# Optimization experiments

Measured on AMD Instinct MI355X. Metric: run time of the kernel, lower is better.

Reference implementation:

```python
import jax, jax.numpy as jnp
import numpy as np

EPS = 1e-5


def _lstm(x, W_ih, W_hh, b_ih, b_hh):
    # x: [B, T, in]; torch LSTM gate order i, f, g, o. Returns (last h, last c).
    def step(carry, xt):
        h, c = carry
        z = xt @ W_ih.T + h @ W_hh.T + (b_ih + b_hh)  # [B, 4H]
        i, f, g, o = jnp.split(z, 4, axis=-1)
        c = jax.nn.sigmoid(f) * c + jax.nn.sigmoid(i) * jnp.tanh(g)
        h = jax.nn.sigmoid(o) * jnp.tanh(c)
        return (h, c), None
    h0 = jnp.zeros((x.shape[0], W_hh.shape[1]), x.dtype)
    (h, c), _ = jax.lax.scan(step, (h0, h0), jnp.swapaxes(x, 0, 1))
    return h, c


def _bn_train(x, g, b):
    # BatchNorm1d in training mode: batch stats, biased variance.
    m = x.mean(axis=0)
    v = x.var(axis=0)
    return g * (x - m) * jax.lax.rsqrt(v + EPS) + b


def _forward(agent_traj, neighbours, aW_ih, aW_hh, ab_ih, ab_hh,
             nW_ih, nW_hh, nb_ih, nb_hh, dW_ih, dW_hh, db_ih, db_hh,
             pW, pb, rW, rb, m1W, m1b, g1, be1, m2W, m2b, g2, be2,
             i1W, i1b, ig1, ib1, i2W, i2b, ig2, ib2, segment_ids):
    B = agent_traj.shape[0]
    # relative distance: neighbour last position - owning agent's last position
    rel = neighbours[:, -1, :] - agent_traj[segment_ids, -1, :]          # [N, 2]
    agent_h, agent_c = _lstm(agent_traj, aW_ih, aW_hh, ab_ih, ab_hh)     # [B, 64]
    neigh_h, _ = _lstm(neighbours, nW_ih, nW_hh, nb_ih, nb_hh)           # [N, 64]
    rel_emb = rel @ rW.T + rb                                            # [N, 64]
    x = jnp.concatenate([neigh_h, rel_emb], axis=1)                      # [N, 128]
    x = _bn_train(jax.nn.relu(x @ m1W.T + m1b), g1, be1)                 # [N, 512]
    x = _bn_train(jax.nn.relu(x @ m2W.T + m2b), g2, be2)                 # [N, 1024]
    # per-sample max pooling over each sample's neighbours (zeros if none)
    pooled = jax.ops.segment_max(x, segment_ids, num_segments=B)         # [B, 1024]
    counts = jax.ops.segment_sum(jnp.ones((x.shape[0],), x.dtype), segment_ids, num_segments=B)
    pooled = jnp.where(counts[:, None] > 0, pooled, jnp.zeros((), x.dtype))
    d = jnp.concatenate([pooled, agent_h], axis=1)                       # [B, 1088]
    d = _bn_train(jax.nn.relu(d @ i1W.T + i1b), ig1, ib1)                # [B, 1024]
    d = _bn_train(jax.nn.relu(d @ i2W.T + i2b), ig2, ib2)                # [B, 64]

    def dec_step(carry, _):
        h, c = carry
        z = h @ dW_ih.T + h @ dW_hh.T + (db_ih + db_hh)
        i, f, g, o = jnp.split(z, 4, axis=-1)
        c = jax.nn.sigmoid(f) * c + jax.nn.sigmoid(i) * jnp.tanh(g)
        h = jax.nn.sigmoid(o) * jnp.tanh(c)
        return (h, c), h
    _, hs = jax.lax.scan(dec_step, (d, agent_c), None, length=30)        # [30, B, 64]
    pred = jnp.einsum('tbh,oh->bto', hs, pW) + pb                        # [B, 30, 2]
    return pred


def setup_inputs() -> dict:
    B, T, N, Tn, H = 2048, 20, 32768, 20, 64
    key = jax.random.key(0)
    ki = iter(jax.random.split(key, 40))
    def rn(shape, s=0.1):
        return jax.random.normal(next(ki), shape, dtype=jnp.float32) * s
    inp = dict(
        agent_traj=rn((B, T, 2), 1.0),
        neighbours=rn((N, Tn, 2), 1.0),
        aW_ih=rn((4 * H, 2)), aW_hh=rn((4 * H, H)), ab_ih=rn((4 * H,)), ab_hh=rn((4 * H,)),
        nW_ih=rn((4 * H, 2)), nW_hh=rn((4 * H, H)), nb_ih=rn((4 * H,)), nb_hh=rn((4 * H,)),
        dW_ih=rn((4 * H, H)), dW_hh=rn((4 * H, H)), db_ih=rn((4 * H,)), db_hh=rn((4 * H,)),
        pW=rn((2, H)), pb=rn((2,)),
        rW=rn((H, 2)), rb=rn((H,)),
        m1W=rn((512, 128)), m1b=rn((512,)),
        g1=jnp.ones((512,), jnp.float32), be1=jnp.zeros((512,), jnp.float32),
        m2W=rn((1024, 512)), m2b=rn((1024,)),
        g2=jnp.ones((1024,), jnp.float32), be2=jnp.zeros((1024,), jnp.float32),
        i1W=rn((1024, 1088)), i1b=rn((1024,)),
        ig1=jnp.ones((1024,), jnp.float32), ib1=jnp.zeros((1024,), jnp.float32),
        i2W=rn((H, 1024)), i2b=rn((H,)),
        ig2=jnp.ones((H,), jnp.float32), ib2=jnp.zeros((H,), jnp.float32),
        segment_ids=jnp.sort(jax.random.randint(next(ki), (N,), 0, B)).astype(jnp.int32),
    )
    return inp


def reference(agent_traj, neighbours, aW_ih, aW_hh, ab_ih, ab_hh,
              nW_ih, nW_hh, nb_ih, nb_hh, dW_ih, dW_hh, db_ih, db_hh,
              pW, pb, rW, rb, m1W, m1b, g1, be1, m2W, m2b, g2, be2,
              i1W, i1b, ig1, ib1, i2W, i2b, ig2, ib2, segment_ids):
    return _forward(agent_traj, neighbours, aW_ih, aW_hh, ab_ih, ab_hh,
                    nW_ih, nW_hh, nb_ih, nb_hh, dW_ih, dW_hh, db_ih, db_hh,
                    pW, pb, rW, rb, m1W, m1b, g1, be1, m2W, m2b, g2, be2,
                    i1W, i1b, ig1, ib1, i2W, i2b, ig2, ib2, segment_ids)
```

## Files before the change

### kernel.cpp

```cpp
#include <hip/hip_runtime.h>

#define EPS_BN 1e-5f

typedef __attribute__((ext_vector_type(8))) short short8;
typedef __attribute__((ext_vector_type(4))) float f32x4;

__device__ __forceinline__ float fast_rcp(float x) { return __builtin_amdgcn_rcpf(x); }
__device__ __forceinline__ float sigmoid_f(float x) { return fast_rcp(1.0f + __expf(-x)); }
__device__ __forceinline__ float tanh_f(float x) { return 1.0f - 2.0f * fast_rcp(__expf(2.0f * x) + 1.0f); }

__device__ __forceinline__ unsigned short f2bf(float f) {
    unsigned u = __float_as_uint(f);
    u += 0x7FFFu + ((u >> 16) & 1u);
    return (unsigned short)(u >> 16);
}
__device__ __forceinline__ unsigned pk_bf(float a, float b) {
    return (unsigned)f2bf(a) | ((unsigned)f2bf(b) << 16);
}
__device__ __forceinline__ float bf_hi(float f) {
    return __uint_as_float((unsigned)f2bf(f) << 16);
}
__device__ __forceinline__ float bf2f(unsigned short u) {
    return __uint_as_float((unsigned)u << 16);
}

union AFrag { short e[8]; short8 v; };
union BFrag { uint4 u; short8 v; };

__global__ __launch_bounds__(256, 2) void lstm_mfma(
    const float* __restrict__ x,
    const float* __restrict__ W_ih,
    const float* __restrict__ W_hh,
    const float* __restrict__ b_ih,
    const float* __restrict__ b_hh,
    float* __restrict__ h_out,
    float* __restrict__ c_out,
    int T)
{
    __shared__ unsigned h_ex[2][16 * 52];
    __shared__ float z_lds[4 * 64 * 17];

    const int tid  = threadIdx.x;
    const int g    = tid >> 6;
    const int lane = tid & 63;
    const int s    = lane & 15;
    const int q    = lane >> 4;

    short8 ahi[4][3], alo[4][3];
#pragma unroll
    for (int Ti = 0; Ti < 4; ++Ti) {
        const int n = g * 64 + Ti * 16 + s;
#pragma unroll
        for (int kc = 0; kc < 2; ++kc) {
            const float* src = &W_hh[n * 64 + kc * 32 + q * 8];
            float4 v0 = *(const float4*)src;
            float4 v1 = *(const float4*)(src + 4);
            float v[8] = {v0.x, v0.y, v0.z, v0.w, v1.x, v1.y, v1.z, v1.w};
            AFrag a, b;
#pragma unroll
            for (int j = 0; j < 8; ++j) {
                a.e[j] = (short)f2bf(v[j]);
                b.e[j] = (short)f2bf(v[j] - bf_hi(v[j]));
            }
            ahi[Ti][kc] = a.v;
            alo[Ti][kc] = b.v;
        }
        AFrag a2, b2;
#pragma unroll
        for (int j = 0; j < 8; ++j) { a2.e[j] = 0; b2.e[j] = 0; }
        if (q == 0) {
            const float wi0 = W_ih[n * 2 + 0];
            const float wi1 = W_ih[n * 2 + 1];
            const float bs  = b_ih[n] + b_hh[n];
            a2.e[0] = (short)f2bf(wi0); b2.e[0] = (short)f2bf(wi0 - bf_hi(wi0));
            a2.e[1] = (short)f2bf(wi1); b2.e[1] = (short)f2bf(wi1 - bf_hi(wi1));
            a2.e[2] = (short)f2bf(bs);  b2.e[2] = (short)f2bf(bs  - bf_hi(bs));
        }
        ahi[Ti][2] = a2.v;
        alo[Ti][2] = b2.v;
    }

    for (int i = tid; i < 2 * 16 * 52; i += 256) (&h_ex[0][0])[i] = 0u;
    __syncthreads();
    if (tid < 16) {
        h_ex[0][tid * 52 + 33] = pk_bf(1.0f, 0.0f);
        float2 xv = *(const float2*)&x[((long)blockIdx.x * 16 + tid) * (long)(T * 2)];
        h_ex[0][tid * 52 + 32] = pk_bf(xv.x, xv.y);
        h_ex[1][tid * 52 + 32] = pk_bf(xv.x - bf_hi(xv.x), xv.y - bf_hi(xv.y));
    }
    __syncthreads();

    const int jg = tid >> 4;
    const int sc = tid & 15;
    const long seqc = (long)blockIdx.x * 16 + sc;
    float creg[4] = {0.f, 0.f, 0.f, 0.f};

    for (int t = 0; t < T; ++t) {
        BFrag bhi[3], blo[3];
#pragma unroll
        for (int kc = 0; kc < 3; ++kc) {
            const int off = s * 52 + kc * 16 + (q >> 1) * 8 + (q & 1) * 4;
            bhi[kc].u = *(const uint4*)&h_ex[0][off];
            blo[kc].u = *(const uint4*)&h_ex[1][off];
        }

        f32x4 acc[4];
#pragma unroll
        for (int Ti = 0; Ti < 4; ++Ti) acc[Ti] = (f32x4)0.f;

#pragma unroll
        for (int kc = 0; kc < 3; ++kc) {
            const short8 bh = bhi[kc].v;
            const short8 bl = blo[kc].v;
#pragma unroll
            for (int Ti = 0; Ti < 4; ++Ti) {
                f32x4 a = acc[Ti];
                a = __builtin_amdgcn_mfma_f32_16x16x32_bf16(ahi[Ti][kc], bh, a, 0, 0, 0);
                a = __builtin_amdgcn_mfma_f32_16x16x32_bf16(ahi[Ti][kc], bl, a, 0, 0, 0);
                a = __builtin_amdgcn_mfma_f32_16x16x32_bf16(alo[Ti][kc], bh, a, 0, 0, 0);
                acc[Ti] = a;
            }
        }

#pragma unroll
        for (int Ti = 0; Ti < 4; ++Ti)
#pragma unroll
        for (int r = 0; r < 4; ++r)
            z_lds[(g * 64 + Ti * 16 + q * 4 + r) * 17 + s] = acc[Ti][r];
        __syncthreads();

        float hval[4];
#pragma unroll
        for (int r = 0; r < 4; ++r) {
            const int j = jg * 4 + r;
            const float zi = z_lds[(0 * 64 + j) * 17 + sc];
            const float zf = z_lds[(1 * 64 + j) * 17 + sc];
            const float zg = z_lds[(2 * 64 + j) * 17 + sc];
            const float zo = z_lds[(3 * 64 + j) * 17 + sc];
            const float c = fmaf(sigmoid_f(zf), creg[r], sigmoid_f(zi) * tanh_f(zg));
            creg[r] = c;
            hval[r] = sigmoid_f(zo) * tanh_f(c);
        }
        {
            const int j0 = jg * 4;
            const int w0 = sc * 52 + (j0 >> 4) * 8 + ((j0 >> 2) & 3) * 2;
            h_ex[0][w0]     = pk_bf(hval[0], hval[1]);
            h_ex[0][w0 + 1] = pk_bf(hval[2], hval[3]);
            h_ex[1][w0]     = pk_bf(hval[0] - bf_hi(hval[0]), hval[1] - bf_hi(hval[1]));
            h_ex[1][w0 + 1] = pk_bf(hval[2] - bf_hi(hval[2]), hval[3] - bf_hi(hval[3]));
        }
        if (tid < 16 && t + 1 < T) {
            float2 xv = *(const float2*)&x[((long)blockIdx.x * 16 + tid) * (long)(T * 2) + (t + 1) * 2];
            h_ex[0][tid * 52 + 32] = pk_bf(xv.x, xv.y);
            h_ex[1][tid * 52 + 32] = pk_bf(xv.x - bf_hi(xv.x), xv.y - bf_hi(xv.y));
        }
        if (t == T - 1) {
#pragma unroll
            for (int r = 0; r < 4; ++r) {
                h_out[seqc * 64 + jg * 4 + r] = hval[r];
                if (c_out) c_out[seqc * 64 + jg * 4 + r] = creg[r];
            }
        }
        __syncthreads();
    }
}

__global__ __launch_bounds__(256) void build_x0(
    const float* __restrict__ neigh_h, const float* __restrict__ neighbours,
    const float* __restrict__ agent_traj, const int* __restrict__ seg,
    const float* __restrict__ rW, const float* __restrict__ rb,
    unsigned short* __restrict__ x0hi, unsigned short* __restrict__ x0lo, int T)
{
    const long n = (long)blockIdx.x * 2 + (threadIdx.x >> 7);
    const int j = threadIdx.x & 127;
    float v;
    if (j < 64) {
        v = neigh_h[n*64 + j];
    } else {
        const int o = j - 64;
        const int sid = seg[n];
        const float ra = neighbours[n*(long)(T*2) + (T-1)*2 + 0] - agent_traj[(long)sid*(T*2) + (T-1)*2 + 0];
        const float rbv= neighbours[n*(long)(T*2) + (T-1)*2 + 1] - agent_traj[(long)sid*(T*2) + (T-1)*2 + 1];
        v = fmaf(rW[o*2+0], ra, fmaf(rW[o*2+1], rbv, rb[o]));
    }
    x0hi[n*128 + j] = f2bf(v);
    x0lo[n*128 + j] = f2bf(v - bf_hi(v));
}

__global__ __launch_bounds__(64) void prep_wfrag(
    const float* __restrict__ W, const float* __restrict__ sc, int K,
    unsigned short* __restrict__ Whi, unsigned short* __restrict__ Wlo)
{
    const int nKc = K >> 5;
    const int blk = blockIdx.x;
    const int ti = blk / nKc, kc = blk - ti * nKc;
    const int l = threadIdx.x;
    const int n = ti * 16 + (l & 15);
    const int k0 = kc * 32 + (l >> 4) * 8;
    const long ob = ((long)blk * 64 + l) * 8;
#pragma unroll
    for (int j = 0; j < 8; ++j) {
        float v = W[(long)n * K + k0 + j];
        if (sc) v *= sc[k0 + j];
        Whi[ob + j] = f2bf(v);
        Wlo[ob + j] = f2bf(v - bf_hi(v));
    }
}

__global__ __launch_bounds__(64) void prep_bias(
    const float* __restrict__ W, const float* __restrict__ sh,
    const float* __restrict__ b, int K, float* __restrict__ bout)
{
    const int n = blockIdx.x;
    const int l = threadIdx.x;
    float s = 0.f;
    if (sh)
        for (int k = l; k < K; k += 64) s += sh[k] * W[(long)n * K + k];
#pragma unroll
    for (int m = 32; m >= 1; m >>= 1) s += __shfl_xor(s, m, 64);
    if (l == 0) bout[n] = b[n] + s;
}

__global__ __launch_bounds__(256, 2) void gemm_split(
    const unsigned short* __restrict__ Ahi,
    const unsigned short* __restrict__ Alo,
    const unsigned short* __restrict__ Whi,
    const unsigned short* __restrict__ Wlo,
    const float* __restrict__ bias,
    float* __restrict__ Yf,
    unsigned short* __restrict__ Yhi,
    unsigned short* __restrict__ Ylo,
    float* __restrict__ accum,
    const int* __restrict__ segp,
    float* __restrict__ poolmax,
    int M, int K, int O)
{
    __shared__ unsigned short As[2][2][128 * 56];
    __shared__ int segl[128];
    const int t = threadIdx.x;
    const int lane = t & 63;
    const int w = t >> 6;
    const int wm = w & 1, wn = w >> 1;

    const int nx = gridDim.x;
    const int flat = blockIdx.y * nx + blockIdx.x;
    const int grp = flat / (8 * nx);
    const int loc = flat - grp * (8 * nx);
    const int m0 = (grp * 8 + (loc & 7)) * 128;
    const int n0 = (loc >> 3) * 128;
    const int nKc = K >> 5;

    f32x4 acc[4][4];
#pragma unroll
    for (int mt = 0; mt < 4; ++mt)
#pragma unroll
    for (int nt = 0; nt < 4; ++nt) acc[mt][nt] = (f32x4)0.f;

    const long aoff = (long)(m0 + (t >> 1)) * K + (t & 1) * 16;
    const unsigned short* aph = Ahi + aoff;
    const unsigned short* apl = Alo + aoff;
    const int so = (t >> 1) * 56 + (t & 1) * 16;
    const int arow = wm * 64 + (lane & 15);
    const int acol = (lane >> 4) * 8;
    const long bt0 = (long)((n0 >> 4) + wn * 4);

    uint4 rah0, rah1, ral0, ral1;
    auto loadAreg = [&](int kc) {
        rah0 = *(const uint4*)(aph + kc * 32);
        rah1 = *(const uint4*)(aph + kc * 32 + 8);
        ral0 = *(const uint4*)(apl + kc * 32);
        ral1 = *(const uint4*)(apl + kc * 32 + 8);
    };
    auto storeAs = [&](int buf) {
        *(uint4*)&As[buf][0][so] = rah0; *(uint4*)&As[buf][0][so + 8] = rah1;
        *(uint4*)&As[buf][1][so] = ral0; *(uint4*)&As[buf][1][so + 8] = ral1;
    };
    auto loadB = [&](BFrag* bh, BFrag* bl, int kc) {
#pragma unroll
        for (int nt = 0; nt < 4; ++nt) {
            const long fb = ((bt0 + nt) * nKc + kc) * 512 + lane * 8;
            bh[nt].u = *(const uint4*)(Whi + fb);
            bl[nt].u = *(const uint4*)(Wlo + fb);
        }
    };
    auto compute = [&](int buf, BFrag* bh, BFrag* bl) {
        BFrag afh[4], afl[4];
#pragma unroll
        for (int mt = 0; mt < 4; ++mt) {
            afh[mt].u = *(const uint4*)&As[buf][0][(arow + mt * 16) * 56 + acol];
            afl[mt].u = *(const uint4*)&As[buf][1][(arow + mt * 16) * 56 + acol];
        }
#pragma unroll
        for (int nt = 0; nt < 4; ++nt)
#pragma unroll
        for (int mt = 0; mt < 4; ++mt) {
            f32x4 a = acc[mt][nt];
            a = __builtin_amdgcn_mfma_f32_16x16x32_bf16(afh[mt].v, bh[nt].v, a, 0, 0, 0);
            a = __builtin_amdgcn_mfma_f32_16x16x32_bf16(afh[mt].v, bl[nt].v, a, 0, 0, 0);
            a = __builtin_amdgcn_mfma_f32_16x16x32_bf16(afl[mt].v, bh[nt].v, a, 0, 0, 0);
            acc[mt][nt] = a;
        }
    };

    BFrag bh0[4], bl0[4], bh1[4], bl1[4];
    loadAreg(0);
    loadB(bh0, bl0, 0);
    storeAs(0);
    __syncthreads();
    for (int kc = 0; kc < nKc; kc += 2) {
        loadAreg(kc + 1);
        loadB(bh1, bl1, kc + 1);
        compute(0, bh0, bl0);
        storeAs(1);
        __syncthreads();
        if (kc + 2 < nKc) {
            loadAreg(kc + 2);
            loadB(bh0, bl0, kc + 2);
        }
        compute(1, bh1, bl1);
        if (kc + 2 < nKc) {
            storeAs(0);
            __syncthreads();
        }
    }

    if (segp) {
        __syncthreads();
        if (t < 128) segl[t] = segp[m0 + t];
        __syncthreads();
    }

    const int cn = lane & 15, cq = lane >> 4;
#pragma unroll
    for (int nt = 0; nt < 4; ++nt) {
        const int n = n0 + wn * 64 + nt * 16 + cn;
        const float bs = bias[n];
        float s = 0.f, ssq = 0.f;
#pragma unroll
        for (int mt = 0; mt < 4; ++mt) {
            const int mb = wm * 64 + mt * 16 + cq * 4;
            float vmax = 0.f; int sid = -1;
#pragma unroll
            for (int r = 0; r < 4; ++r) {
                const float v = fmaxf(acc[mt][nt][r] + bs, 0.f);
                s += v; ssq += v * v;
                if (segp) {
                    const int sr = segl[mb + r];
                    if (r == 0) { vmax = v; sid = sr; }
                    else if (sr == sid) { vmax = fmaxf(vmax, v); }
                    else {
                        if (vmax > 0.f)
                            atomicMax((int*)&poolmax[(long)sid * O + n], __float_as_int(vmax));
                        sid = sr; vmax = v;
                    }
                } else if (Yf) {
                    Yf[(long)(m0 + mb + r) * O + n] = v;
                } else {
                    const long idx = (long)(m0 + mb + r) * O + n;
                    Yhi[idx] = f2bf(v);
                    Ylo[idx] = f2bf(v - bf_hi(v));
                }
            }
            if (segp && vmax > 0.f)
                atomicMax((int*)&poolmax[(long)sid * O + n], __float_as_int(vmax));
        }
        if (accum) {
            s   += __shfl_xor(s, 16, 64);   ssq += __shfl_xor(ssq, 16, 64);
            s   += __shfl_xor(s, 32, 64);   ssq += __shfl_xor(ssq, 32, 64);
            if (cq == 0) {
                atomicAdd(&accum[n], s);
                atomicAdd(&accum[O + n], ssq);
            }
        }
    }
}

__global__ __launch_bounds__(256) void colstats(
    const float* __restrict__ Y, int M, int O, int chunkRows,
    float* __restrict__ accum)
{
    const int c = blockIdx.x * 64 + (threadIdx.x & 63);
    const int rgrp = threadIdx.x >> 6;
    const int r0 = blockIdx.y * chunkRows;
    int rend = r0 + chunkRows; if (rend > M) rend = M;
    float s = 0.f, ss = 0.f;
    for (int r = r0 + rgrp; r < rend; r += 4) {
        const float v = Y[(long)r*O + c];
        s += v; ss += v*v;
    }
    __shared__ float l1[256], l2[256];
    l1[threadIdx.x] = s; l2[threadIdx.x] = ss;
    __syncthreads();
    if (threadIdx.x < 64) {
        const int c2 = blockIdx.x * 64 + threadIdx.x;
        s  = l1[threadIdx.x] + l1[threadIdx.x+64] + l1[threadIdx.x+128] + l1[threadIdx.x+192];
        ss = l2[threadIdx.x] + l2[threadIdx.x+64] + l2[threadIdx.x+128] + l2[threadIdx.x+192];
        atomicAdd(&accum[c2], s);
        atomicAdd(&accum[O + c2], ss);
    }
}

__global__ __launch_bounds__(256) void bn_finalize(
    const float* __restrict__ accum, const float* __restrict__ g,
    const float* __restrict__ be, int O, float invM,
    float* __restrict__ scale, float* __restrict__ shift)
{
    const int o = blockIdx.x * 256 + threadIdx.x;
    if (o < O) {
        const float mean = accum[o] * invM;
        const float var  = accum[O + o] * invM - mean * mean;
        const float sc   = g[o] * rsqrtf(var + EPS_BN);
        scale[o] = sc;
        shift[o] = be[o] - mean * sc;
    }
}

__global__ __launch_bounds__(256) void build_d0(
    const float* __restrict__ poolraw, const float* __restrict__ agent_h,
    const int* __restrict__ seg, int N,
    const float* __restrict__ sc2, const float* __restrict__ sh2,
    unsigned short* __restrict__ d0hi, unsigned short* __restrict__ d0lo)
{
    const int b = blockIdx.x;
    int l = 0, h = N;
    while (l < h) { const int mid = (l + h) >> 1; if (seg[mid] < b) l = mid + 1; else h = mid; }
    const bool nonempty = (l < N) && (seg[l] == b);
    for (int c = threadIdx.x; c < 1088; c += 256) {
        float v;
        if (c < 1024) {
            v = nonempty ? fmaf(sc2[c], poolraw[(long)b*1024 + c], sh2[c]) : 0.f;
        } else {
            v = agent_h[(long)b*64 + (c - 1024)];
        }
        d0hi[(long)b*1088 + c] = f2bf(v);
        d0lo[(long)b*1088 + c] = f2bf(v - bf_hi(v));
    }
}

__global__ __launch_bounds__(256) void gemm_i2_part(
    const float* __restrict__ A,
    const float* __restrict__ W,
    const float* __restrict__ ascale, const float* __restrict__ ashift,
    float* __restrict__ part, int M, int K, int kchunk)
{
    __shared__ float As[16][132];
    __shared__ float Bs[16][68];
    const int t = threadIdx.x;
    const int m0 = blockIdx.x * 128;
    const int ks = blockIdx.y;
    const int kbeg = ks * kchunk;
    const int kend = kbeg + kchunk;
    const int tm = (t & 15) * 8;
    const int tn = (t >> 4) * 4;
    const int ar = t >> 1;
    const int ac = (t & 1) * 8;
    const int br = t >> 2;
    const int bc = (t & 3) * 4;

    float acc[8][4];
#pragma unroll
    for (int i = 0; i < 8; ++i)
#pragma unroll
    for (int j = 0; j < 4; ++j) acc[i][j] = 0.f;

    for (int k0 = kbeg; k0 < kend; k0 += 16) {
        float4 a0 = *(const float4*)&A[(long)(m0+ar)*K + k0 + ac];
        float4 a1 = *(const float4*)&A[(long)(m0+ar)*K + k0 + ac + 4];
        float4 s0 = *(const float4*)&ascale[k0 + ac];
        float4 s1 = *(const float4*)&ascale[k0 + ac + 4];
        float4 h0 = *(const float4*)&ashift[k0 + ac];
        float4 h1 = *(const float4*)&ashift[k0 + ac + 4];
        a0.x = fmaf(a0.x, s0.x, h0.x); a0.y = fmaf(a0.y, s0.y, h0.y);
        a0.z = fmaf(a0.z, s0.z, h0.z); a0.w = fmaf(a0.w, s0.w, h0.w);
        a1.x = fmaf(a1.x, s1.x, h1.x); a1.y = fmaf(a1.y, s1.y, h1.y);
        a1.z = fmaf(a1.z, s1.z, h1.z); a1.w = fmaf(a1.w, s1.w, h1.w);
        float4 b0 = *(const float4*)&W[(long)br*K + k0 + bc];
        __syncthreads();
        As[ac+0][ar] = a0.x; As[ac+1][ar] = a0.y; As[ac+2][ar] = a0.z; As[ac+3][ar] = a0.w;
        As[ac+4][ar] = a1.x; As[ac+5][ar] = a1.y; As[ac+6][ar] = a1.z; As[ac+7][ar] = a1.w;
        Bs[bc+0][br] = b0.x; Bs[bc+1][br] = b0.y; Bs[bc+2][br] = b0.z; Bs[bc+3][br] = b0.w;
        __syncthreads();
#pragma unroll
        for (int kk = 0; kk < 16; ++kk) {
            float av[8], bv[4];
            *(float4*)&av[0] = *(const float4*)&As[kk][tm];
            *(float4*)&av[4] = *(const float4*)&As[kk][tm + 4];
            *(float4*)&bv[0] = *(const float4*)&Bs[kk][tn];
#pragma unroll
            for (int i = 0; i < 8; ++i)
#pragma unroll
            for (int j = 0; j < 4; ++j)
                acc[i][j] = fmaf(av[i], bv[j], acc[i][j]);
        }
    }

    float* po = part + (long)ks * M * 64;
#pragma unroll
    for (int i = 0; i < 8; ++i)
        *(float4*)&po[(long)(m0 + tm + i) * 64 + tn] = *(float4*)&acc[i][0];
}

__global__ __launch_bounds__(256) void i2_finish(
    const float* __restrict__ part, const float* __restrict__ bias,
    int M, int KS, float* __restrict__ t2)
{
    const long idx = (long)blockIdx.x * 256 + threadIdx.x;
    if (idx < (long)M * 64) {
        float s = 0.f;
        for (int ks = 0; ks < KS; ++ks) s += part[(long)ks * M * 64 + idx];
        t2[idx] = fmaxf(s + bias[idx & 63], 0.f);
    }
}

__global__ __launch_bounds__(256) void prep_dec(
    const float* __restrict__ dW_ih, const float* __restrict__ dW_hh,
    const float* __restrict__ db_ih, const float* __restrict__ db_hh,
    float* __restrict__ Wc, float* __restrict__ bc)
{
    const int idx = blockIdx.x * 256 + threadIdx.x;
    if (idx < 256*64) Wc[idx] = dW_ih[idx] + dW_hh[idx];
    else if (idx < 256*64 + 256) bc[idx - 256*64] = db_ih[idx - 256*64] + db_hh[idx - 256*64];
}

__global__ __launch_bounds__(256) void decoder_kernel(
    const float* __restrict__ t2, const float* __restrict__ sc4,
    const float* __restrict__ sh4, const float* __restrict__ agent_c,
    const float* __restrict__ Wc, const float* __restrict__ bc,
    const float* __restrict__ pW, const float* __restrict__ pb,
    float* __restrict__ pred )
{
    __shared__ float h_lds[2][64];
    __shared__ float zg_lds[2][64];
    __shared__ float zo_lds[2][64];
    const int t = threadIdx.x;
    const int lane = t & 63;
    const int wave = t >> 6;
    const int s = wave >> 1;
    const int role = wave & 1;
    const long seq = (long)blockIdx.x * 2 + s;

    const int r0 = role * 128 + lane;
    const int r1 = r0 + 64;
    float w0[64], w1[64];
#pragma unroll
    for (int k = 0; k < 64; k += 4) {
        float4 va = *(const float4*)&Wc[r0 * 64 + k];
        w0[k] = va.x; w0[k+1] = va.y; w0[k+2] = va.z; w0[k+3] = va.w;
        float4 vb = *(const float4*)&Wc[r1 * 64 + k];
        w1[k] = vb.x; w1[k+1] = vb.y; w1[k+2] = vb.z; w1[k+3] = vb.w;
    }
    const float bias0 = bc[r0];
    const float bias1 = bc[r1];
    const float pw0 = pW[lane], pw1 = pW[64 + lane];
    const float pb0 = pb[0], pb1 = pb[1];

    float c = agent_c[seq*64 + lane];
    if (role == 0)
        h_lds[s][lane] = fmaf(sc4[lane], t2[seq*64 + lane], sh4[lane]);
    __syncthreads();
    float hv = h_lds[s][lane];

    for (int step = 0; step < 30; ++step) {
        float z0 = bias0, z1 = bias1;
#pragma unroll
        for (int k = 0; k < 64; ++k) {
            float hk = __int_as_float(__builtin_amdgcn_readlane(__float_as_int(hv), k));
            z0 = fmaf(hk, w0[k], z0);
            z1 = fmaf(hk, w1[k], z1);
        }
        if (role == 1) { zg_lds[s][lane] = z0; zo_lds[s][lane] = z1; }
        __syncthreads();
        if (role == 0) {
            const float ig = sigmoid_f(z0);
            const float fg = sigmoid_f(z1);
            const float gg = tanh_f(zg_lds[s][lane]);
            const float og = sigmoid_f(zo_lds[s][lane]);
            c = fmaf(fg, c, ig * gg);
            h_lds[s][lane] = og * tanh_f(c);
        }
        __syncthreads();
        hv = h_lds[s][lane];
        if (role == 0) {
            float p0 = hv * pw0;
            float p1 = hv * pw1;
#pragma unroll
            for (int m = 32; m >= 1; m >>= 1) {
                p0 += __shfl_xor(p0, m, 64);
                p1 += __shfl_xor(p1, m, 64);
            }
            if (lane == 0) {
                pred[seq*60 + step*2 + 0] = p0 + pb0;
                pred[seq*60 + step*2 + 1] = p1 + pb1;
            }
        }
    }
}

extern "C" void kernel_launch(void* const* d_in, const int* in_sizes, int n_in,
                              void* d_out, int out_size, void* d_ws, size_t ws_size,
                              hipStream_t stream)
{
    const float* agent_traj = (const float*)d_in[0];
    const float* neighbours = (const float*)d_in[1];
    const float* aW_ih = (const float*)d_in[2];
    const float* aW_hh = (const float*)d_in[3];
    const float* ab_ih = (const float*)d_in[4];
    const float* ab_hh = (const float*)d_in[5];
    const float* nW_ih = (const float*)d_in[6];
    const float* nW_hh = (const float*)d_in[7];
    const float* nb_ih = (const float*)d_in[8];
    const float* nb_hh = (const float*)d_in[9];
    const float* dW_ih = (const float*)d_in[10];
    const float* dW_hh = (const float*)d_in[11];
    const float* db_ih = (const float*)d_in[12];
    const float* db_hh = (const float*)d_in[13];
    const float* pW = (const float*)d_in[14];
    const float* pb = (const float*)d_in[15];
    const float* rW = (const float*)d_in[16];
    const float* rb = (const float*)d_in[17];
    const float* m1W = (const float*)d_in[18];
    const float* m1b = (const float*)d_in[19];
    const float* g1  = (const float*)d_in[20];
    const float* be1 = (const float*)d_in[21];
    const float* m2W = (const float*)d_in[22];
    const float* m2b = (const float*)d_in[23];
    const float* g2  = (const float*)d_in[24];
    const float* be2 = (const float*)d_in[25];
    const float* i1W = (const float*)d_in[26];
    const float* i1b = (const float*)d_in[27];
    const float* ig1 = (const float*)d_in[28];
    const float* ib1 = (const float*)d_in[29];
    const float* i2W = (const float*)d_in[30];
    const float* i2b = (const float*)d_in[31];
    const float* ig2 = (const float*)d_in[32];
    const float* ib2 = (const float*)d_in[33];
    const int*   seg = (const int*)d_in[34];
    float* pred = (float*)d_out;

    const int B = 2048, T = 20, N = 32768;

    char* p = (char*)d_ws;
    auto alloc = [&](size_t bytes) -> char* {
        char* r = p; p += (bytes + 255) & ~(size_t)255; return r;
    };
    float* agent_h = (float*)alloc((size_t)B*64*4);
    float* agent_c = (float*)alloc((size_t)B*64*4);
    char* neigh_region = alloc((size_t)N*64*4);
    unsigned short* x0hi = (unsigned short*)alloc((size_t)N*128*2);
    unsigned short* x0lo = (unsigned short*)alloc((size_t)N*128*2);
    char* y1hi_region  = alloc((size_t)N*512*2);
    unsigned short* y1lo = (unsigned short*)alloc((size_t)N*512*2);
    float* poolraw = (float*)alloc((size_t)B*1024*4);
    float* accAll = (float*)alloc((size_t)(1024+2048+2048+128)*4);
    float* acc1 = accAll;
    float* acc2 = accAll + 1024;
    float* acc3 = accAll + 3072;
    float* acc4 = accAll + 5120;
    float* sc1 = (float*)alloc(512*4);  float* sh1 = (float*)alloc(512*4);
    float* sc2 = (float*)alloc(1024*4); float* sh2 = (float*)alloc(1024*4);
    float* sc3 = (float*)alloc(1024*4); float* sh3 = (float*)alloc(1024*4);
    float* sc4 = (float*)alloc(64*4);   float* sh4 = (float*)alloc(64*4);
    float* Wc = (float*)alloc(256*64*4);
    float* bc = (float*)alloc(256*4);
    unsigned short* W1hi = (unsigned short*)alloc((size_t)512*128*2);
    unsigned short* W1lo = (unsigned short*)alloc((size_t)512*128*2);
    unsigned short* W2hi = (unsigned short*)alloc((size_t)1024*512*2);
    unsigned short* W2lo = (unsigned short*)alloc((size_t)1024*512*2);
    unsigned short* Wi1hi = (unsigned short*)alloc((size_t)1024*1088*2);
    unsigned short* Wi1lo = (unsigned short*)alloc((size_t)1024*1088*2);
    float* b1f = (float*)alloc(512*4);
    float* b2f = (float*)alloc(1024*4);
    float* bi1f = (float*)alloc(1024*4);
    float* i2part = (float*)alloc((size_t)8*B*64*4);

    float* neigh_h = (float*)neigh_region;
    float* t1      = (float*)neigh_region;
    unsigned short* y1hi = (unsigned short*)y1hi_region;
    unsigned short* d0hi = (unsigned short*)y1hi_region;
    unsigned short* d0lo = d0hi + (size_t)B*1088;
    float* t2 = (float*)(y1hi_region + (size_t)2*B*1088*2);

    hipMemsetAsync(accAll, 0, (1024+2048+2048+128)*sizeof(float), stream);
    hipMemsetAsync(poolraw, 0, (size_t)B*1024*4, stream);

    prep_wfrag<<<(512/16)*(128/32), 64, 0, stream>>>(m1W, nullptr, 128, W1hi, W1lo);
    prep_bias<<<512, 64, 0, stream>>>(m1W, nullptr, m1b, 128, b1f);
    prep_wfrag<<<(1024/16)*(1088/32), 64, 0, stream>>>(i1W, nullptr, 1088, Wi1hi, Wi1lo);
    prep_bias<<<1024, 64, 0, stream>>>(i1W, nullptr, i1b, 1088, bi1f);
    prep_dec<<<65, 256, 0, stream>>>(dW_ih, dW_hh, db_ih, db_hh, Wc, bc);

    lstm_mfma<<<B/16, 256, 0, stream>>>(agent_traj, aW_ih, aW_hh, ab_ih, ab_hh,
                                        agent_h, agent_c, T);
    lstm_mfma<<<N/16, 256, 0, stream>>>(neighbours, nW_ih, nW_hh, nb_ih, nb_hh,
                                        neigh_h, nullptr, T);
    build_x0<<<N/2, 256, 0, stream>>>(neigh_h, neighbours, agent_traj, seg, rW, rb,
                                      x0hi, x0lo, T);

    gemm_split<<<dim3(512/128, N/128), 256, 0, stream>>>(
        x0hi, x0lo, W1hi, W1lo, b1f, nullptr, y1hi, y1lo, acc1,
        nullptr, nullptr, N, 128, 512);
    bn_finalize<<<2, 256, 0, stream>>>(acc1, g1, be1, 512, 1.0f/N, sc1, sh1);

    prep_wfrag<<<(1024/16)*(512/32), 64, 0, stream>>>(m2W, sc1, 512, W2hi, W2lo);
    prep_bias<<<1024, 64, 0, stream>>>(m2W, sh1, m2b, 512, b2f);

    gemm_split<<<dim3(1024/128, N/128), 256, 0, stream>>>(
        y1hi, y1lo, W2hi, W2lo, b2f, nullptr, nullptr, nullptr, acc2,
        seg, poolraw, N, 512, 1024);
    bn_finalize<<<4, 256, 0, stream>>>(acc2, g2, be2, 1024, 1.0f/N, sc2, sh2);

    build_d0<<<B, 256, 0, stream>>>(poolraw, agent_h, seg, N, sc2, sh2, d0hi, d0lo);

    gemm_split<<<dim3(1024/128, B/128), 256, 0, stream>>>(
        d0hi, d0lo, Wi1hi, Wi1lo, bi1f, t1, nullptr, nullptr, acc3,
        nullptr, nullptr, B, 1088, 1024);
    bn_finalize<<<4, 256, 0, stream>>>(acc3, ig1, ib1, 1024, 1.0f/B, sc3, sh3);

    gemm_i2_part<<<dim3(B/128, 8), 256, 0, stream>>>(t1, i2W, sc3, sh3, i2part,
                                                     B, 1024, 128);
    i2_finish<<<(B*64)/256, 256, 0, stream>>>(i2part, i2b, B, 8, t2);
    colstats<<<dim3(1, 8), 256, 0, stream>>>(t2, B, 64, 256, acc4);
    bn_finalize<<<1, 256, 0, stream>>>(acc4, ig2, ib2, 64, 1.0f/B, sc4, sh4);

    decoder_kernel<<<B/2, 256, 0, stream>>>(t2, sc4, sh4, agent_c, Wc, bc, pW, pb, pred);
}
```

Before: 648.5 us.

## Remap LSTM gate rows per wave to drop LDS z-exchange and barrier

Reassigns weight rows so each wave owns the i, f, g and o gate rows for the same 16 hidden units. The cell update can then be computed directly from MFMA accumulators, with no round trip through z_lds and no __syncthreads. The h exchange buffer is double-buffered, so only one barrier per timestep remains, and the final h/c stores become float4. The aim is to cut LDS traffic and synchronisation on the serial recurrence critical path, at the cost of doubling the h_ex buffer.

```diff
diff --git a/kernel.cpp b/kernel.cpp
--- a/kernel.cpp
+++ b/kernel.cpp
@@ -37,19 +37,18 @@
     float* __restrict__ c_out,
     int T)
 {
-    __shared__ unsigned h_ex[2][16 * 52];
-    __shared__ float z_lds[4 * 64 * 17];
+    __shared__ unsigned h_ex[2][2][16 * 52];
 
     const int tid  = threadIdx.x;
-    const int g    = tid >> 6;
+    const int w    = tid >> 6;
     const int lane = tid & 63;
     const int s    = lane & 15;
     const int q    = lane >> 4;
 
     short8 ahi[4][3], alo[4][3];
 #pragma unroll
-    for (int Ti = 0; Ti < 4; ++Ti) {
-        const int n = g * 64 + Ti * 16 + s;
+    for (int gt = 0; gt < 4; ++gt) {
+        const int n = gt * 64 + w * 16 + s;
 #pragma unroll
         for (int kc = 0; kc < 2; ++kc) {
             const float* src = &W_hh[n * 64 + kc * 32 + q * 8];
@@ -62,8 +61,8 @@
                 a.e[j] = (short)f2bf(v[j]);
                 b.e[j] = (short)f2bf(v[j] - bf_hi(v[j]));
             }
-            ahi[Ti][kc] = a.v;
-            alo[Ti][kc] = b.v;
+            ahi[gt][kc] = a.v;
+            alo[gt][kc] = b.v;
         }
         AFrag a2, b2;
 #pragma unroll
@@ -76,90 +75,77 @@
             a2.e[1] = (short)f2bf(wi1); b2.e[1] = (short)f2bf(wi1 - bf_hi(wi1));
             a2.e[2] = (short)f2bf(bs);  b2.e[2] = (short)f2bf(bs  - bf_hi(bs));
         }
-        ahi[Ti][2] = a2.v;
-        alo[Ti][2] = b2.v;
-    }
-
-    for (int i = tid; i < 2 * 16 * 52; i += 256) (&h_ex[0][0])[i] = 0u;
+        ahi[gt][2] = a2.v;
+        alo[gt][2] = b2.v;
+    }
+
+    for (int i = tid; i < 2 * 2 * 16 * 52; i += 256) (&h_ex[0][0][0])[i] = 0u;
     __syncthreads();
     if (tid < 16) {
-        h_ex[0][tid * 52 + 33] = pk_bf(1.0f, 0.0f);
+        h_ex[0][0][tid * 52 + 33] = pk_bf(1.0f, 0.0f);
+        h_ex[1][0][tid * 52 + 33] = pk_bf(1.0f, 0.0f);
         float2 xv = *(const float2*)&x[((long)blockIdx.x * 16 + tid) * (long)(T * 2)];
-        h_ex[0][tid * 52 + 32] = pk_bf(xv.x, xv.y);
-        h_ex[1][tid * 52 + 32] = pk_bf(xv.x - bf_hi(xv.x), xv.y - bf_hi(xv.y));
+        h_ex[0][0][tid * 52 + 32] = pk_bf(xv.x, xv.y);
+        h_ex[0][1][tid * 52 + 32] = pk_bf(xv.x - bf_hi(xv.x), xv.y - bf_hi(xv.y));
     }
     __syncthreads();
 
-    const int jg = tid >> 4;
-    const int sc = tid & 15;
-    const long seqc = (long)blockIdx.x * 16 + sc;
     float creg[4] = {0.f, 0.f, 0.f, 0.f};
 
     for (int t = 0; t < T; ++t) {
+        const int rb = t & 1, wb = rb ^ 1;
         BFrag bhi[3], blo[3];
 #pragma unroll
         for (int kc = 0; kc < 3; ++kc) {
             const int off = s * 52 + kc * 16 + (q >> 1) * 8 + (q & 1) * 4;
-            bhi[kc].u = *(const uint4*)&h_ex[0][off];
-            blo[kc].u = *(const uint4*)&h_ex[1][off];
+            bhi[kc].u = *(const uint4*)&h_ex[rb][0][off];
+            blo[kc].u = *(const uint4*)&h_ex[rb][1][off];
         }
 
         f32x4 acc[4];
 #pragma unroll
-        for (int Ti = 0; Ti < 4; ++Ti) acc[Ti] = (f32x4)0.f;
+        for (int gt = 0; gt < 4; ++gt) acc[gt] = (f32x4)0.f;
 
 #pragma unroll
         for (int kc = 0; kc < 3; ++kc) {
             const short8 bh = bhi[kc].v;
             const short8 bl = blo[kc].v;
 #pragma unroll
-            for (int Ti = 0; Ti < 4; ++Ti) {
-                f32x4 a = acc[Ti];
-                a = __builtin_amdgcn_mfma_f32_16x16x32_bf16(ahi[Ti][kc], bh, a, 0, 0, 0);
-                a = __builtin_amdgcn_mfma_f32_16x16x32_bf16(ahi[Ti][kc], bl, a, 0, 0, 0);
-                a = __builtin_amdgcn_mfma_f32_16x16x32_bf16(alo[Ti][kc], bh, a, 0, 0, 0);
-                acc[Ti] = a;
+            for (int gt = 0; gt < 4; ++gt) {
+                f32x4 a = acc[gt];
+                a = __builtin_amdgcn_mfma_f32_16x16x32_bf16(ahi[gt][kc], bh, a, 0, 0, 0);
+                a = __builtin_amdgcn_mfma_f32_16x16x32_bf16(ahi[gt][kc], bl, a, 0, 0, 0);
+                a = __builtin_amdgcn_mfma_f32_16x16x32_bf16(alo[gt][kc], bh, a, 0, 0, 0);
+                acc[gt] = a;
             }
         }
 
-#pragma unroll
-        for (int Ti = 0; Ti < 4; ++Ti)
-#pragma unroll
-        for (int r = 0; r < 4; ++r)
-            z_lds[(g * 64 + Ti * 16 + q * 4 + r) * 17 + s] = acc[Ti][r];
-        __syncthreads();
-
         float hval[4];
 #pragma unroll
         for (int r = 0; r < 4; ++r) {
-            const int j = jg * 4 + r;
-            const float zi = z_lds[(0 * 64 + j) * 17 + sc];
-            const float zf = z_lds[(1 * 64 + j) * 17 + sc];
-            const float zg = z_lds[(2 * 64 + j) * 17 + sc];
-            const float zo = z_lds[(3 * 64 + j) * 17 + sc];
-            const float c = fmaf(sigmoid_f(zf), creg[r], sigmoid_f(zi) * tanh_f(zg));
+            const float c = fmaf(sigmoid_f(acc[1][r]), creg[r],
+                                 sigmoid_f(acc[0][r]) * tanh_f(acc[2][r]));
             creg[r] = c;
-            hval[r] = sigmoid_f(zo) * tanh_f(c);
+            hval[r] = sigmoid_f(acc[3][r]) * tanh_f(c);
         }
         {
-            const int j0 = jg * 4;
-            const int w0 = sc * 52 + (j0 >> 4) * 8 + ((j0 >> 2) & 3) * 2;
-            h_ex[0][w0]     = pk_bf(hval[0], hval[1]);
-            h_ex[0][w0 + 1] = pk_bf(hval[2], hval[3]);
-            h_ex[1][w0]     = pk_bf(hval[0] - bf_hi(hval[0]), hval[1] - bf_hi(hval[1]));
-            h_ex[1][w0 + 1] = pk_bf(hval[2] - bf_hi(hval[2]), hval[3] - bf_hi(hval[3]));
+            const int w0 = s * 52 + w * 8 + q * 2;
+            h_ex[wb][0][w0]     = pk_bf(hval[0], hval[1]);
+            h_ex[wb][0][w0 + 1] = pk_bf(hval[2], hval[3]);
+            h_ex[wb][1][w0]     = pk_bf(hval[0] - bf_hi(hval[0]), hval[1] - bf_hi(hval[1]));
+            h_ex[wb][1][w0 + 1] = pk_bf(hval[2] - bf_hi(hval[2]), hval[3] - bf_hi(hval[3]));
         }
         if (tid < 16 && t + 1 < T) {
             float2 xv = *(const float2*)&x[((long)blockIdx.x * 16 + tid) * (long)(T * 2) + (t + 1) * 2];
-            h_ex[0][tid * 52 + 32] = pk_bf(xv.x, xv.y);
-            h_ex[1][tid * 52 + 32] = pk_bf(xv.x - bf_hi(xv.x), xv.y - bf_hi(xv.y));
+            h_ex[wb][0][tid * 52 + 32] = pk_bf(xv.x, xv.y);
+            h_ex[wb][1][tid * 52 + 32] = pk_bf(xv.x - bf_hi(xv.x), xv.y - bf_hi(xv.y));
         }
         if (t == T - 1) {
-#pragma unroll
-            for (int r = 0; r < 4; ++r) {
-                h_out[seqc * 64 + jg * 4 + r] = hval[r];
-                if (c_out) c_out[seqc * 64 + jg * 4 + r] = creg[r];
-            }
+            const long seq = (long)blockIdx.x * 16 + s;
+            const int j0 = w * 16 + q * 4;
+            *(float4*)&h_out[seq * 64 + j0] = make_float4(hval[0], hval[1], hval[2], hval[3]);
+            if (c_out)
+                *(float4*)&c_out[seq * 64 + j0] = make_float4(creg[0], creg[1], creg[2], creg[3]);
         }
         __syncthreads();
     }
```

New measurement: 641.4 us (median of 2 runs). No clear change (-1.1%).
